# Performance work log

Measured on AMD Instinct MI355X. Metric: run time of the kernel, lower is better.

Reference implementation:

```python
import jax, jax.numpy as jnp
import numpy as np

N_NODES = 50000
N_EDGES = 800000
N_FEAT = 128
N_CLASSES = 64
K_HOPS = 2


def setup_inputs() -> dict:
    key = jax.random.key(0)
    k1, k2, k3, k4 = jax.random.split(key, 4)
    x = jax.random.normal(k1, (N_NODES, N_FEAT), dtype=jnp.float32)
    edge_index = jax.random.randint(k2, (2, N_EDGES), 0, N_NODES, dtype=jnp.int64)
    # Linear(num_features -> num_classes) params (PyG SGConv lin layer)
    lim = 1.0 / np.sqrt(N_FEAT)
    W = jax.random.uniform(k3, (N_CLASSES, N_FEAT), minval=-lim, maxval=lim, dtype=jnp.float32)
    b = jax.random.uniform(k4, (N_CLASSES,), minval=-lim, maxval=lim, dtype=jnp.float32)
    return {"x": x, "edge_index": edge_index, "W": W, "b": b}


def reference(x, edge_index, W, b):
    N = x.shape[0]
    # gcn_norm: add self-loops, symmetric normalization deg^-1/2 A_hat deg^-1/2
    loop = jnp.arange(N, dtype=edge_index.dtype)
    src = jnp.concatenate([edge_index[0], loop])  # message sources j
    dst = jnp.concatenate([edge_index[1], loop])  # message targets i
    deg = jax.ops.segment_sum(jnp.ones_like(src, dtype=x.dtype), dst, num_segments=N)
    dinv = jnp.where(deg > 0, jax.lax.rsqrt(deg), 0.0)
    norm = dinv[src] * dinv[dst]  # [E+N]
    # K=2 hops of SpMM: out[i] = sum_{j->i} norm * x[j]
    for _ in range(K_HOPS):
        x = jax.ops.segment_sum(norm[:, None] * x[src], dst, num_segments=N)
    logits = x @ W.T + b  # [N, num_classes]
    return jax.nn.log_softmax(logits, axis=1)
```

## Files before the change

### kernel.cpp

```cpp
#include <hip/hip_runtime.h>
#include <hip/hip_fp16.h>
#include <math.h>

#define NFEAT 128
#define NCLS  64
#define RQ8   8
#define WSTR  132
#define NBLK  256
#define BSLACK 2048


typedef _Float16 h2v __attribute__((ext_vector_type(2)));

__device__ __forceinline__ float dot2acc(unsigned int hv, unsigned int wv, float c) {
#if __has_builtin(__builtin_amdgcn_fdot2)
    union { unsigned int u; h2v v; } a, bq; a.u = hv; bq.u = wv;
    return __builtin_amdgcn_fdot2(a.v, bq.v, c, false);
#else
    union { unsigned int u; __half2 h; } a, bq; a.u = hv; bq.u = wv;
    float2 fa = __half22float2(a.h), fb = __half22float2(bq.h);
    return fmaf(fa.x, fb.x, fmaf(fa.y, fb.y, c));
#endif
}

__device__ __forceinline__ void acc4(__half2 a[4], uint4 v) {
    union { uint4 u; __half2 h[4]; } c; c.u = v;
    a[0] = __hadd2(a[0], c.h[0]); a[1] = __hadd2(a[1], c.h[1]);
    a[2] = __hadd2(a[2], c.h[2]); a[3] = __hadd2(a[3], c.h[3]);
}

__device__ __forceinline__ __half2 red8(__half2 a) {
    union { __half2 h; int i; } u, v;
    u.h = a; v.i = __shfl_xor(u.i, 8);  a = __hadd2(a, v.h);
    u.h = a; v.i = __shfl_xor(u.i, 16); a = __hadd2(a, v.h);
    u.h = a; v.i = __shfl_xor(u.i, 32); a = __hadd2(a, v.h);
    return a;
}

__device__ __forceinline__ int block_excl_scan_256(int v, int tid, int* scratch, int* total) {
    const int lane = tid & 63, wv = tid >> 6;
    __syncthreads();
    int x = v;
    #pragma unroll
    for (int off = 1; off < 64; off <<= 1) {
        int y = __shfl_up(x, off);
        if (lane >= off) x += y;
    }
    if (lane == 63) scratch[wv] = x;
    __syncthreads();
    if (wv == 0 && lane < 4) {
        int t = scratch[lane];
        int y = __shfl_up(t, 1); if (lane >= 1) t += y;
        y = __shfl_up(t, 2);     if (lane >= 2) t += y;
        scratch[4 + lane] = t;
    }
    __syncthreads();
    int wbase = (wv == 0) ? 0 : scratch[4 + wv - 1];
    if (total) *total = scratch[7];
    return wbase + x - v;
}

__global__ __launch_bounds__(256) void hist_kernel(const int* __restrict__ dst,
                                                   int* __restrict__ h,
                                                   int E4, int E, int nb) {
    __shared__ int lh[256];
    const int tid = threadIdx.x;
    lh[tid] = 0;
    __syncthreads();
    for (int idx = blockIdx.x * 256 + tid; idx < E4; idx += NBLK * 256) {
        int base = idx * 4;
        if (base + 3 < E) {
            int4 d = ((const int4*)dst)[idx];
            atomicAdd(&lh[d.x >> 8], 1); atomicAdd(&lh[d.y >> 8], 1);
            atomicAdd(&lh[d.z >> 8], 1); atomicAdd(&lh[d.w >> 8], 1);
        } else {
            for (int e = base; e < E; ++e) atomicAdd(&lh[dst[e] >> 8], 1);
        }
    }
    __syncthreads();
    if (tid < nb) h[blockIdx.x * nb + tid] = lh[tid];
}

__global__ __launch_bounds__(256) void colscan_kernel(int* __restrict__ h,
                                                      int* __restrict__ btot, int nb) {
    __shared__ int scratch[8];
    const int tid = threadIdx.x;
    const int B = blockIdx.x;
    int v = h[tid * nb + B];
    int tot;
    int pre = block_excl_scan_256(v, tid, scratch, &tot);
    h[tid * nb + B] = pre;
    if (tid == 0) btot[B] = tot;
}

__global__ __launch_bounds__(256) void bucket_scatter_kernel(const int* __restrict__ src,
                                                             const int* __restrict__ dst,
                                                             const int* __restrict__ h,
                                                             const int* __restrict__ btot,
                                                             unsigned int* __restrict__ bedg,
                                                             int E4, int E, int nb) {
    __shared__ int cur[256];
    __shared__ int scratch[8];
    const int tid = threadIdx.x;
    int bt = (tid < nb) ? btot[tid] : 0;
    int pre = block_excl_scan_256(bt, tid, scratch, nullptr);
    if (tid < nb) cur[tid] = pre + h[blockIdx.x * nb + tid];
    __syncthreads();
    for (int idx = blockIdx.x * 256 + tid; idx < E4; idx += NBLK * 256) {
        int base = idx * 4;
        if (base + 3 < E) {
            int4 s = ((const int4*)src)[idx];
            int4 d = ((const int4*)dst)[idx];
            int p;
            p = atomicAdd(&cur[d.x >> 8], 1); bedg[p] = ((unsigned)s.x << 8) | (d.x & 255);
            p = atomicAdd(&cur[d.y >> 8], 1); bedg[p] = ((unsigned)s.y << 8) | (d.y & 255);
            p = atomicAdd(&cur[d.z >> 8], 1); bedg[p] = ((unsigned)s.z << 8) | (d.z & 255);
            p = atomicAdd(&cur[d.w >> 8], 1); bedg[p] = ((unsigned)s.w << 8) | (d.w & 255);
        } else {
            for (int e = base; e < E; ++e) {
                int p = atomicAdd(&cur[dst[e] >> 8], 1);
                bedg[p] = ((unsigned)src[e] << 8) | (dst[e] & 255);
            }
        }
    }
}

__global__ __launch_bounds__(256) void drain_kernel(const unsigned int* __restrict__ bedg,
                                                    const int* __restrict__ btot,
                                                    int* __restrict__ csr,
                                                    int* __restrict__ rbeg,
                                                    int* __restrict__ rend,
                                                    float* __restrict__ dinv,
                                                    int N, int nb) {
    __shared__ int lcnt[256];
    __shared__ int loc[256];
    __shared__ int scratch[8];
    __shared__ int s0_s, s1_s;
    const int B = blockIdx.x;
    const int tid = threadIdx.x;

    int bt = (tid < nb) ? btot[tid] : 0;
    int pre = block_excl_scan_256(bt, tid, scratch, nullptr);
    if (tid == B) { s0_s = pre; s1_s = pre + bt; }
    lcnt[tid] = 0;
    __syncthreads();
    const int s0 = s0_s, s1 = s1_s;

    for (int e = s0 + tid; e < s1; e += 256)
        atomicAdd(&lcnt[bedg[e] & 255u], 1);
    __syncthreads();

    const int c = lcnt[tid];
    const int cp = (c + 8) & ~7;
    int rpre = block_excl_scan_256(cp, tid, scratch, nullptr);
    const int base = s0 + BSLACK * B;
    loc[tid] = base + rpre;
    __syncthreads();
    lcnt[tid] = loc[tid];
    __syncthreads();

    for (int e = s0 + tid; e < s1; e += 256) {
        unsigned int Ev = bedg[e];
        int p = atomicAdd(&lcnt[Ev & 255u], 1);
        csr[p] = (int)(Ev >> 8);
    }
    __syncthreads();

    int i = B * 256 + tid;
    if (i < N) {
        int start = loc[tid], end = start + cp;
        int q = lcnt[tid];
        csr[q++] = i;
        for (int p = q; p < end; ++p) csr[p] = N;
        rbeg[i] = start; rend[i] = end;
        dinv[i] = rsqrtf((float)c + 1.0f);
    }
}

__global__ __launch_bounds__(512) void gemm_kernel(const float* __restrict__ x,
                                                   const float* __restrict__ W,
                                                   const float* __restrict__ dinv,
                                                   __half* __restrict__ zh,
                                                   __half* __restrict__ y1h, int N) {
    __shared__ __half Wl[NCLS * WSTR];
    __shared__ __align__(16) __half HT[64][NFEAT];

    const int tid = threadIdx.x;
    const int w = tid >> 6, lane = tid & 63;

    if (blockIdx.x == 0 && tid < 32) {
        if (tid < 16) ((uint2*)zh)[(size_t)N * 16 + tid] = uint2{0u, 0u};
        else          ((uint2*)y1h)[(size_t)N * 16 + (tid - 16)] = uint2{0u, 0u};
    }

    for (int e = tid; e < NCLS * NFEAT; e += 512) {
        int r = e >> 7, c = e & 127;
        Wl[r * WSTR + c] = __float2half(W[e]);
    }
    {
        const float4* srcf = (const float4*)(x + (size_t)blockIdx.x * 64 * NFEAT);
        uint2* dh = (uint2*)&HT[0][0];
        const int row0 = blockIdx.x * 64;
        #pragma unroll
        for (int t = 0; t < 4; ++t) {
            int e = tid + 512 * t;
            float4 f = (row0 + (e >> 5) < N) ? srcf[e] : float4{0.f, 0.f, 0.f, 0.f};
            union { uint2 u; __half2 h[2]; } r;
            r.h[0] = __floats2half2_rn(f.x, f.y);
            r.h[1] = __floats2half2_rn(f.z, f.w);
            dh[e] = r.u;
        }
    }
    __syncthreads();

    unsigned int wreg[64];
    {
        const uint2* wr = (const uint2*)&Wl[lane * WSTR];
        #pragma unroll
        for (int t = 0; t < 32; ++t) {
            uint2 v = wr[t];
            wreg[2 * t] = v.x; wreg[2 * t + 1] = v.y;
        }
    }

    #pragma unroll 1
    for (int r = 0; r < 8; ++r) {
        int node = blockIdx.x * 64 + w * 8 + r;
        if (node >= N) break;
        const unsigned int* hrow = (const unsigned int*)&HT[w * 8 + r][0];
        float dot = 0.f;
        #pragma unroll
        for (int t = 0; t < 64; ++t)
            dot = dot2acc(hrow[t], wreg[t], dot);
        zh[(size_t)node * NCLS + lane] = __float2half(dinv[node] * dot);
    }
}

__device__ __forceinline__ void gather_row64(__half2 a[4], const uint4* __restrict__ X,
                                             const int* __restrict__ csr,
                                             int ks, int ke, int sub, int q, int Nd) {
    int k = ks;
    int j0, j1, j2, j3;
    bool have = (k + 32 <= ke);
    if (have) {
        j0 = csr[k + sub];      j1 = csr[k + 8 + sub];
        j2 = csr[k + 16 + sub]; j3 = csr[k + 24 + sub];
    }
    while (have) {
        uint4 v0 = X[(size_t)j0 * RQ8 + q];
        uint4 v1 = X[(size_t)j1 * RQ8 + q];
        uint4 v2 = X[(size_t)j2 * RQ8 + q];
        uint4 v3 = X[(size_t)j3 * RQ8 + q];
        k += 32;
        have = (k + 32 <= ke);
        if (have) {
            j0 = csr[k + sub];      j1 = csr[k + 8 + sub];
            j2 = csr[k + 16 + sub]; j3 = csr[k + 24 + sub];
        }
        acc4(a, v0); acc4(a, v1); acc4(a, v2); acc4(a, v3);
    }
    int rem = (ke - k) >> 3;
    if (rem) {
        int t0 = csr[k + sub];
        int t1 = csr[k + 8 + sub];
        int t2 = csr[k + 16 + sub];
        if (rem < 2) t1 = Nd;
        if (rem < 3) t2 = Nd;
        uint4 v0 = X[(size_t)t0 * RQ8 + q];
        uint4 v1 = X[(size_t)t1 * RQ8 + q];
        uint4 v2 = X[(size_t)t2 * RQ8 + q];
        acc4(a, v0); acc4(a, v1); acc4(a, v2);
    }
}

template <int SQUARE>
__global__ __launch_bounds__(256) void hop64_kernel(const __half* __restrict__ in_h,
                                                    const float* __restrict__ dinv,
                                                    const int* __restrict__ rbeg,
                                                    const int* __restrict__ rend,
                                                    const int* __restrict__ csr,
                                                    __half* __restrict__ out_h, int N) {
    const int tid = threadIdx.x;
    const int w = tid >> 6, lane = tid & 63;
    const int i = blockIdx.x * 4 + w;
    if (i >= N) return;
    const int sub = lane >> 3;
    const int q = lane & 7;
    const uint4* X = (const uint4*)in_h;

    __half2 a[4];
    a[0] = __float2half2_rn(0.f); a[1] = a[0]; a[2] = a[0]; a[3] = a[0];

    int ks = rbeg[i], ke = rend[i];
    gather_row64(a, X, csr, ks, ke, sub, q, N);

    a[0] = red8(a[0]); a[1] = red8(a[1]); a[2] = red8(a[2]); a[3] = red8(a[3]);

    if (sub == 0) {
        float di = dinv[i];
        float s = SQUARE ? di * di : di;
        union { uint4 u; __half2 h[4]; } r;
        #pragma unroll
        for (int t = 0; t < 4; ++t) {
            float2 f = __half22float2(a[t]);
            r.h[t] = __floats2half2_rn(s * f.x, s * f.y);
        }
        ((uint4*)out_h)[(size_t)i * RQ8 + q] = r.u;
    }
}

__global__ __launch_bounds__(256) void hop2cls_kernel(const __half* __restrict__ in_h,
                                                      const float* __restrict__ dinv,
                                                      const int* __restrict__ rbeg,
                                                      const int* __restrict__ rend,
                                                      const int* __restrict__ csr,
                                                      const float* __restrict__ b,
                                                      float* __restrict__ out, int N) {
    const int tid = threadIdx.x;
    const int w = tid >> 6, lane = tid & 63;
    const int i = blockIdx.x * 4 + w;
    if (i >= N) return;
    const int sub = lane >> 3;
    const int q = lane & 7;
    const uint4* X = (const uint4*)in_h;

    float4 b0 = ((const float4*)b)[q * 2];
    float4 b1 = ((const float4*)b)[q * 2 + 1];

    __half2 a[4];
    a[0] = __float2half2_rn(0.f); a[1] = a[0]; a[2] = a[0]; a[3] = a[0];

    int ks = rbeg[i], ke = rend[i];
    gather_row64(a, X, csr, ks, ke, sub, q, N);

    a[0] = red8(a[0]); a[1] = red8(a[1]); a[2] = red8(a[2]); a[3] = red8(a[3]);

    if (sub == 0) {
        float di = dinv[i];
        float f[8];
        float2 p;
        p = __half22float2(a[0]); f[0] = fmaf(di, p.x, b0.x); f[1] = fmaf(di, p.y, b0.y);
        p = __half22float2(a[1]); f[2] = fmaf(di, p.x, b0.z); f[3] = fmaf(di, p.y, b0.w);
        p = __half22float2(a[2]); f[4] = fmaf(di, p.x, b1.x); f[5] = fmaf(di, p.y, b1.y);
        p = __half22float2(a[3]); f[6] = fmaf(di, p.x, b1.z); f[7] = fmaf(di, p.y, b1.w);
        float m = f[0];
        #pragma unroll
        for (int t = 1; t < 8; ++t) m = fmaxf(m, f[t]);
        m = fmaxf(m, __shfl_xor(m, 1));
        m = fmaxf(m, __shfl_xor(m, 2));
        m = fmaxf(m, __shfl_xor(m, 4));
        float se = 0.f;
        #pragma unroll
        for (int t = 0; t < 8; ++t) se += __expf(f[t] - m);
        se += __shfl_xor(se, 1);
        se += __shfl_xor(se, 2);
        se += __shfl_xor(se, 4);
        float ls = m + logf(se);
        float4 o0 = {f[0] - ls, f[1] - ls, f[2] - ls, f[3] - ls};
        float4 o1 = {f[4] - ls, f[5] - ls, f[6] - ls, f[7] - ls};
        float4* op = (float4*)(out + (size_t)i * NCLS);
        op[q * 2] = o0; op[q * 2 + 1] = o1;
    }
}


static inline size_t align256(size_t v) { return (v + 255) & ~(size_t)255; }

extern "C" void kernel_launch(void* const* d_in, const int* in_sizes, int n_in,
                              void* d_out, int out_size, void* d_ws, size_t ws_size,
                              hipStream_t stream) {
    const float* x  = (const float*)d_in[0];
    const int*   ei = (const int*)d_in[1];
    const float* W  = (const float*)d_in[2];
    const float* b  = (const float*)d_in[3];
    float* out = (float*)d_out;

    const int N = in_sizes[0] / NFEAT;
    const int E = in_sizes[1] / 2;
    const int* src = ei;
    const int* dst = ei + E;
    const int NBUCK = (N + 255) >> 8;

    const int CSR_CAP = E + BSLACK * NBUCK + 64;

    char* ws = (char*)d_ws;
    size_t o = 0;
    int*          h     = (int*)(ws + o);          o += align256((size_t)NBLK * NBUCK * 4);
    int*          btot  = (int*)(ws + o);          o += align256(256 * 4);
    unsigned int* bedg  = (unsigned int*)(ws + o); o += align256((size_t)E * 4);
    int*          csr   = (int*)(ws + o);          o += align256((size_t)CSR_CAP * 4);
    int*          rbeg  = (int*)(ws + o);          o += align256((size_t)N * 4);
    int*          rend  = (int*)(ws + o);          o += align256((size_t)N * 4);
    float*        dinv  = (float*)(ws + o);        o += align256((size_t)N * 4);
    __half*       zh    = (__half*)(ws + o);       o += align256((size_t)(N + 1) * NCLS * 2);
    __half*       y1h   = (__half*)(ws + o);       o += align256((size_t)(N + 1) * NCLS * 2);

    const int E4 = (E + 3) / 4;

    hist_kernel<<<NBLK, 256, 0, stream>>>(dst, h, E4, E, NBUCK);
    colscan_kernel<<<NBUCK, 256, 0, stream>>>(h, btot, NBUCK);
    bucket_scatter_kernel<<<NBLK, 256, 0, stream>>>(src, dst, h, btot, bedg, E4, E, NBUCK);
    drain_kernel<<<NBUCK, 256, 0, stream>>>(bedg, btot, csr, rbeg, rend, dinv, N, NBUCK);
    gemm_kernel<<<(N + 63) / 64, 512, 0, stream>>>(x, W, dinv, zh, y1h, N);
    hop64_kernel<1><<<(N + 3) / 4, 256, 0, stream>>>(zh, dinv, rbeg, rend, csr, y1h, N);
    hop2cls_kernel<<<(N + 3) / 4, 256, 0, stream>>>(y1h, dinv, rbeg, rend, csr, b, out, N);
}
```

Before: 155.8 us.

## Split CSR rows by source-node half to improve gather cache locality

Each destination row's neighbor list is split into two padded segments, one for sources in the lower half of the node range and one for the upper half. Each SpMM hop then runs as two passes, so each pass gathers from only half of the feature table, which is meant to fit better in L2/MALL. The partial sum from the first pass is kept in an fp16 buffer and reloaded by the second pass. This adds two kernel launches, extra partial-sum traffic, more padding per row, and a larger slack per bucket in the CSR.

```diff
diff --git a/kernel.cpp b/kernel.cpp
--- a/kernel.cpp
+++ b/kernel.cpp
@@ -7,7 +7,7 @@
 #define RQ8   8
 #define WSTR  132
 #define NBLK  256
-#define BSLACK 2048
+#define BSLACK 8192
 
 
 typedef _Float16 h2v __attribute__((ext_vector_type(2)));
@@ -129,11 +129,12 @@
                                                     const int* __restrict__ btot,
                                                     int* __restrict__ csr,
                                                     int* __restrict__ rbeg,
+                                                    int* __restrict__ rmid,
                                                     int* __restrict__ rend,
                                                     float* __restrict__ dinv,
-                                                    int N, int nb) {
-    __shared__ int lcnt[256];
-    __shared__ int loc[256];
+                                                    int N, int nb, int halfN) {
+    __shared__ int lcnt0[256];
+    __shared__ int lcnt1[256];
     __shared__ int scratch[8];
     __shared__ int s0_s, s1_s;
     const int B = blockIdx.x;
@@ -142,38 +143,50 @@
     int bt = (tid < nb) ? btot[tid] : 0;
     int pre = block_excl_scan_256(bt, tid, scratch, nullptr);
     if (tid == B) { s0_s = pre; s1_s = pre + bt; }
-    lcnt[tid] = 0;
+    lcnt0[tid] = 0; lcnt1[tid] = 0;
     __syncthreads();
     const int s0 = s0_s, s1 = s1_s;
-
-    for (int e = s0 + tid; e < s1; e += 256)
-        atomicAdd(&lcnt[bedg[e] & 255u], 1);
-    __syncthreads();
-
-    const int c = lcnt[tid];
-    const int cp = (c + 8) & ~7;
-    int rpre = block_excl_scan_256(cp, tid, scratch, nullptr);
-    const int base = s0 + BSLACK * B;
-    loc[tid] = base + rpre;
-    __syncthreads();
-    lcnt[tid] = loc[tid];
-    __syncthreads();
 
     for (int e = s0 + tid; e < s1; e += 256) {
         unsigned int Ev = bedg[e];
-        int p = atomicAdd(&lcnt[Ev & 255u], 1);
-        csr[p] = (int)(Ev >> 8);
-    }
-    __syncthreads();
-
-    int i = B * 256 + tid;
-    if (i < N) {
-        int start = loc[tid], end = start + cp;
-        int q = lcnt[tid];
-        csr[q++] = i;
-        for (int p = q; p < end; ++p) csr[p] = N;
-        rbeg[i] = start; rend[i] = end;
-        dinv[i] = rsqrtf((float)c + 1.0f);
+        int d = Ev & 255u;
+        if ((int)(Ev >> 8) < halfN) atomicAdd(&lcnt0[d], 1);
+        else                        atomicAdd(&lcnt1[d], 1);
+    }
+    __syncthreads();
+
+    const int i = B * 256 + tid;
+    const bool valid = (i < N);
+    const int c0 = lcnt0[tid], c1 = lcnt1[tid];
+    const bool selfLo = (i < halfN);
+    const int cp0 = valid ? (((c0 + (selfLo ? 1 : 0)) + 7) & ~7) : 0;
+    const int cp1 = valid ? (((c1 + (selfLo ? 0 : 1)) + 7) & ~7) : 0;
+    int rpre = block_excl_scan_256(cp0 + cp1, tid, scratch, nullptr);
+    const int start = s0 + BSLACK * B + rpre;
+    __syncthreads();
+    lcnt0[tid] = start;
+    lcnt1[tid] = start + cp0;
+    __syncthreads();
+
+    for (int e = s0 + tid; e < s1; e += 256) {
+        unsigned int Ev = bedg[e];
+        int d = Ev & 255u, s = (int)(Ev >> 8);
+        int p = atomicAdd((s < halfN) ? &lcnt0[d] : &lcnt1[d], 1);
+        csr[p] = s;
+    }
+    __syncthreads();
+
+    if (valid) {
+        int st = start;
+        int mid = st + cp0, end = mid + cp1;
+        int q0 = lcnt0[tid];
+        if (selfLo) csr[q0++] = i;
+        for (int p = q0; p < mid; ++p) csr[p] = N;
+        int q1 = lcnt1[tid];
+        if (!selfLo) csr[q1++] = i;
+        for (int p = q1; p < end; ++p) csr[p] = N;
+        rbeg[i] = st; rmid[i] = mid; rend[i] = end;
+        dinv[i] = rsqrtf((float)(c0 + c1) + 1.0f);
     }
 }
 
@@ -262,10 +275,8 @@
     int rem = (ke - k) >> 3;
     if (rem) {
         int t0 = csr[k + sub];
-        int t1 = csr[k + 8 + sub];
-        int t2 = csr[k + 16 + sub];
-        if (rem < 2) t1 = Nd;
-        if (rem < 3) t2 = Nd;
+        int t1 = (rem >= 2) ? csr[k + 8 + sub]  : Nd;
+        int t2 = (rem >= 3) ? csr[k + 16 + sub] : Nd;
         uint4 v0 = X[(size_t)t0 * RQ8 + q];
         uint4 v1 = X[(size_t)t1 * RQ8 + q];
         uint4 v2 = X[(size_t)t2 * RQ8 + q];
@@ -273,13 +284,11 @@
     }
 }
 
-template <int SQUARE>
-__global__ __launch_bounds__(256) void hop64_kernel(const __half* __restrict__ in_h,
-                                                    const float* __restrict__ dinv,
-                                                    const int* __restrict__ rbeg,
-                                                    const int* __restrict__ rend,
-                                                    const int* __restrict__ csr,
-                                                    __half* __restrict__ out_h, int N) {
+__global__ __launch_bounds__(256) void hop_lo_kernel(const __half* __restrict__ in_h,
+                                                     const int* __restrict__ rbeg,
+                                                     const int* __restrict__ rmid,
+                                                     const int* __restrict__ csr,
+                                                     __half* __restrict__ part, int N) {
     const int tid = threadIdx.x;
     const int w = tid >> 6, lane = tid & 63;
     const int i = blockIdx.x * 4 + w;
@@ -291,31 +300,24 @@
     __half2 a[4];
     a[0] = __float2half2_rn(0.f); a[1] = a[0]; a[2] = a[0]; a[3] = a[0];
 
-    int ks = rbeg[i], ke = rend[i];
-    gather_row64(a, X, csr, ks, ke, sub, q, N);
+    gather_row64(a, X, csr, rbeg[i], rmid[i], sub, q, N);
 
     a[0] = red8(a[0]); a[1] = red8(a[1]); a[2] = red8(a[2]); a[3] = red8(a[3]);
 
     if (sub == 0) {
-        float di = dinv[i];
-        float s = SQUARE ? di * di : di;
         union { uint4 u; __half2 h[4]; } r;
-        #pragma unroll
-        for (int t = 0; t < 4; ++t) {
-            float2 f = __half22float2(a[t]);
-            r.h[t] = __floats2half2_rn(s * f.x, s * f.y);
-        }
-        ((uint4*)out_h)[(size_t)i * RQ8 + q] = r.u;
-    }
-}
-
-__global__ __launch_bounds__(256) void hop2cls_kernel(const __half* __restrict__ in_h,
+        r.h[0] = a[0]; r.h[1] = a[1]; r.h[2] = a[2]; r.h[3] = a[3];
+        ((uint4*)part)[(size_t)i * RQ8 + q] = r.u;
+    }
+}
+
+__global__ __launch_bounds__(256) void hop1_hi_kernel(const __half* __restrict__ in_h,
+                                                      const __half* __restrict__ part,
                                                       const float* __restrict__ dinv,
-                                                      const int* __restrict__ rbeg,
+                                                      const int* __restrict__ rmid,
                                                       const int* __restrict__ rend,
                                                       const int* __restrict__ csr,
-                                                      const float* __restrict__ b,
-                                                      float* __restrict__ out, int N) {
+                                                      __half* __restrict__ out_h, int N) {
     const int tid = threadIdx.x;
     const int w = tid >> 6, lane = tid & 63;
     const int i = blockIdx.x * 4 + w;
@@ -324,14 +326,61 @@
     const int q = lane & 7;
     const uint4* X = (const uint4*)in_h;
 
+    __half2 a[4];
+    if (sub == 0) {
+        union { uint4 u; __half2 h[4]; } c;
+        c.u = ((const uint4*)part)[(size_t)i * RQ8 + q];
+        a[0] = c.h[0]; a[1] = c.h[1]; a[2] = c.h[2]; a[3] = c.h[3];
+    } else {
+        a[0] = __float2half2_rn(0.f); a[1] = a[0]; a[2] = a[0]; a[3] = a[0];
+    }
+
+    gather_row64(a, X, csr, rmid[i], rend[i], sub, q, N);
+
+    a[0] = red8(a[0]); a[1] = red8(a[1]); a[2] = red8(a[2]); a[3] = red8(a[3]);
+
+    if (sub == 0) {
+        float di = dinv[i];
+        float s = di * di;
+        union { uint4 u; __half2 h[4]; } r;
+        #pragma unroll
+        for (int t = 0; t < 4; ++t) {
+            float2 f = __half22float2(a[t]);
+            r.h[t] = __floats2half2_rn(s * f.x, s * f.y);
+        }
+        ((uint4*)out_h)[(size_t)i * RQ8 + q] = r.u;
+    }
+}
+
+__global__ __launch_bounds__(256) void hop2cls_hi_kernel(const __half* __restrict__ in_h,
+                                                         const __half* __restrict__ part,
+                                                         const float* __restrict__ dinv,
+                                                         const int* __restrict__ rmid,
+                                                         const int* __restrict__ rend,
+                                                         const int* __restrict__ csr,
+                                                         const float* __restrict__ b,
+                                                         float* __restrict__ out, int N) {
+    const int tid = threadIdx.x;
+    const int w = tid >> 6, lane = tid & 63;
+    const int i = blockIdx.x * 4 + w;
+    if (i >= N) return;
+    const int sub = lane >> 3;
+    const int q = lane & 7;
+    const uint4* X = (const uint4*)in_h;
+
     float4 b0 = ((const float4*)b)[q * 2];
     float4 b1 = ((const float4*)b)[q * 2 + 1];
 
     __half2 a[4];
-    a[0] = __float2half2_rn(0.f); a[1] = a[0]; a[2] = a[0]; a[3] = a[0];
-
-    int ks = rbeg[i], ke = rend[i];
-    gather_row64(a, X, csr, ks, ke, sub, q, N);
+    if (sub == 0) {
+        union { uint4 u; __half2 h[4]; } c;
+        c.u = ((const uint4*)part)[(size_t)i * RQ8 + q];
+        a[0] = c.h[0]; a[1] = c.h[1]; a[2] = c.h[2]; a[3] = c.h[3];
+    } else {
+        a[0] = __float2half2_rn(0.f); a[1] = a[0]; a[2] = a[0]; a[3] = a[0];
+    }
+
+    gather_row64(a, X, csr, rmid[i], rend[i], sub, q, N);
 
     a[0] = red8(a[0]); a[1] = red8(a[1]); a[2] = red8(a[2]); a[3] = red8(a[3]);
 
@@ -380,6 +429,7 @@
     const int* src = ei;
     const int* dst = ei + E;
     const int NBUCK = (N + 255) >> 8;
+    const int halfN = (N + 1) >> 1;
 
     const int CSR_CAP = E + BSLACK * NBUCK + 64;
 
@@ -390,18 +440,24 @@
     unsigned int* bedg  = (unsigned int*)(ws + o); o += align256((size_t)E * 4);
     int*          csr   = (int*)(ws + o);          o += align256((size_t)CSR_CAP * 4);
     int*          rbeg  = (int*)(ws + o);          o += align256((size_t)N * 4);
+    int*          rmid  = (int*)(ws + o);          o += align256((size_t)N * 4);
     int*          rend  = (int*)(ws + o);          o += align256((size_t)N * 4);
     float*        dinv  = (float*)(ws + o);        o += align256((size_t)N * 4);
     __half*       zh    = (__half*)(ws + o);       o += align256((size_t)(N + 1) * NCLS * 2);
     __half*       y1h   = (__half*)(ws + o);       o += align256((size_t)(N + 1) * NCLS * 2);
+    __half*       part  = (__half*)(ws + o);       o += align256((size_t)N * NCLS * 2);
 
     const int E4 = (E + 3) / 4;
+    const int HG = (N + 3) / 4;
 
     hist_kernel<<<NBLK, 256, 0, stream>>>(dst, h, E4, E, NBUCK);
     colscan_kernel<<<NBUCK, 256, 0, stream>>>(h, btot, NBUCK);
     bucket_scatter_kernel<<<NBLK, 256, 0, stream>>>(src, dst, h, btot, bedg, E4, E, NBUCK);
-    drain_kernel<<<NBUCK, 256, 0, stream>>>(bedg, btot, csr, rbeg, rend, dinv, N, NBUCK);
+    drain_kernel<<<NBUCK, 256, 0, stream>>>(bedg, btot, csr, rbeg, rmid, rend, dinv,
+                                            N, NBUCK, halfN);
     gemm_kernel<<<(N + 63) / 64, 512, 0, stream>>>(x, W, dinv, zh, y1h, N);
-    hop64_kernel<1><<<(N + 3) / 4, 256, 0, stream>>>(zh, dinv, rbeg, rend, csr, y1h, N);
-    hop2cls_kernel<<<(N + 3) / 4, 256, 0, stream>>>(y1h, dinv, rbeg, rend, csr, b, out, N);
-}
+    hop_lo_kernel<<<HG, 256, 0, stream>>>(zh, rbeg, rmid, csr, part, N);
+    hop1_hi_kernel<<<HG, 256, 0, stream>>>(zh, part, dinv, rmid, rend, csr, y1h, N);
+    hop_lo_kernel<<<HG, 256, 0, stream>>>(y1h, rbeg, rmid, csr, part, N);
+    hop2cls_hi_kernel<<<HG, 256, 0, stream>>>(y1h, part, dinv, rmid, rend, csr, b, out, N);
+}
```

After: 184.0 us. 18.1% more time.
